# Optimization experiments

Measured on AMD Instinct MI355X. Metric: run time of the kernel, lower is better.

Reference implementation:

```python
import jax, jax.numpy as jnp
import numpy as np

B, L, D = 2, 4096, 128      # batch, seq_len, d_model
ED = 2 * D                  # d_inner (expand=2) = 256
N = 16                      # d_state
K = 4                       # d_conv
R = (D + 15) // 16          # dt_rank = 8
H = 2 * D                   # mlp hidden = 256


def setup_inputs() -> dict:
    key = jax.random.key(0)
    ks = jax.random.split(key, 20)
    s = 0.05
    inp = {
        "x": jax.random.normal(ks[0], (B, L, D), dtype=jnp.float32),
        # outer block LayerNorm (norm1)
        "norm1_g": jnp.ones((D,), jnp.float32),
        "norm1_b": jnp.zeros((D,), jnp.float32),
        # MambaLayer inner LayerNorm
        "inner_g": jnp.ones((D,), jnp.float32),
        "inner_b": jnp.zeros((D,), jnp.float32),
        # Mamba params
        "in_w": jax.random.normal(ks[1], (2 * ED, D), jnp.float32) * s,      # in_proj (no bias)
        "conv_w": jax.random.normal(ks[2], (ED, 1, K), jnp.float32) * s,     # depthwise conv
        "conv_b": jax.random.normal(ks[3], (ED,), jnp.float32) * s,
        "xproj_w": jax.random.normal(ks[4], (R + 2 * N, ED), jnp.float32) * s,  # x_proj (no bias)
        "dt_w": jax.random.normal(ks[5], (ED, R), jnp.float32) * s,
        "dt_b": jax.random.normal(ks[6], (ED,), jnp.float32) * s,
        "A_log": jnp.tile(jnp.log(jnp.arange(1, N + 1, dtype=jnp.float32)), (ED, 1)),  # [ED,N]
        "Dp": jnp.ones((ED,), jnp.float32),
        "out_w": jax.random.normal(ks[7], (D, ED), jnp.float32) * s,         # out_proj (no bias)
        # MLP
        "fc1_w": jax.random.normal(ks[8], (H, D), jnp.float32) * s,
        "fc1_b": jnp.zeros((H,), jnp.float32),
        "fc2_w": jax.random.normal(ks[9], (D, H), jnp.float32) * s,
        "fc2_b": jnp.zeros((D,), jnp.float32),
    }
    return inp


def _ln(x, g, b, eps=1e-5):
    m = jnp.mean(x, axis=-1, keepdims=True)
    v = jnp.mean((x - m) ** 2, axis=-1, keepdims=True)
    return (x - m) * jax.lax.rsqrt(v + eps) * g + b


def _mamba(x, in_w, conv_w, conv_b, xproj_w, dt_w, dt_b, A_log, Dp, out_w):
    # x: [B, L, D]
    xz = jnp.einsum('bld,ed->ble', x, in_w)          # [B,L,2*ED]
    u, z = jnp.split(xz, 2, axis=-1)                 # each [B,L,ED]
    # causal depthwise conv1d over L
    u_c = jnp.transpose(u, (0, 2, 1))                # [B,ED,L]
    u_c = jax.lax.conv_general_dilated(
        u_c, conv_w, window_strides=(1,), padding=[(K - 1, 0)],
        dimension_numbers=('NCH', 'OIH', 'NCH'), feature_group_count=ED)
    u = jax.nn.silu(jnp.transpose(u_c, (0, 2, 1)) + conv_b)   # [B,L,ED]
    # input-dependent dt, B, C
    dbc = jnp.einsum('ble,re->blr', u, xproj_w)      # [B,L,R+2N]
    dt, Bm, Cm = jnp.split(dbc, [R, R + N], axis=-1)
    delta = jax.nn.softplus(jnp.einsum('blr,er->ble', dt, dt_w) + dt_b)  # [B,L,ED]
    A = -jnp.exp(A_log)                              # [ED,N]
    deltaA = jnp.exp(jnp.einsum('ble,en->blen', delta, A))               # [B,L,ED,N]
    deltaBu = jnp.einsum('ble,bln,ble->blen', delta, Bm, u)              # [B,L,ED,N]
    # selective scan over L
    def step(h, inp):
        dA, dBu, Ct = inp                            # [B,ED,N],[B,ED,N],[B,N]
        h = dA * h + dBu
        y = jnp.einsum('ben,bn->be', h, Ct)
        return h, y
    h0 = jnp.zeros((B, ED, N), u.dtype)
    xs = (jnp.transpose(deltaA, (1, 0, 2, 3)),
          jnp.transpose(deltaBu, (1, 0, 2, 3)),
          jnp.transpose(Cm, (1, 0, 2)))
    _, ys = jax.lax.scan(step, h0, xs)               # [L,B,ED]
    y = jnp.transpose(ys, (1, 0, 2)) + u * Dp        # [B,L,ED]
    y = y * jax.nn.silu(z)
    return jnp.einsum('ble,de->bld', y, out_w)       # [B,L,D]


def reference(x, norm1_g, norm1_b, inner_g, inner_b, in_w, conv_w, conv_b,
              xproj_w, dt_w, dt_b, A_log, Dp, out_w, fc1_w, fc1_b, fc2_w, fc2_b):
    # attn branch: mamba(inner_LN(norm1(x)))
    a = _mamba(_ln(_ln(x, norm1_g, norm1_b), inner_g, inner_b),
               in_w, conv_w, conv_b, xproj_w, dt_w, dt_b, A_log, Dp, out_w)
    x = x + a
    # mlp branch (note: original applies norm1 again to updated x)
    h = _ln(x, norm1_g, norm1_b)
    h = jax.nn.gelu(jnp.einsum('bld,hd->blh', h, fc1_w) + fc1_b, approximate=False)
    h = jnp.einsum('blh,dh->bld', h, fc2_w) + fc2_b
    return x + h
```

## Files before the change

### kernel.cpp

```cpp
#include <hip/hip_runtime.h>
#include <hip/hip_bf16.h>
#include <math.h>

#define BB 2
#define LL 4096
#define DD 128
#define ED 256
#define NN 16
#define KK 4
#define RR 8
#define HH 256
#define NT (BB*LL)
#define NC 128
#define LC 32

typedef __attribute__((ext_vector_type(8))) short short8;
typedef __attribute__((ext_vector_type(8))) unsigned short ushort8v;
typedef __attribute__((ext_vector_type(4))) float floatx4;

__device__ __forceinline__ unsigned short f2bf(float f) {
  unsigned int b = __builtin_bit_cast(unsigned int, f);
  b += 0x7FFFu + ((b >> 16) & 1u);
  return (unsigned short)(b >> 16);
}

__global__ __launch_bounds__(256) void cvt5_k(const float* __restrict__ a,
    const float* __restrict__ b, const float* __restrict__ c,
    const float* __restrict__ d, const float* __restrict__ e5,
    unsigned short* __restrict__ oa, unsigned short* __restrict__ ob,
    unsigned short* __restrict__ oc, unsigned short* __restrict__ od,
    unsigned short* __restrict__ oe) {
  const int i = blockIdx.x*256 + threadIdx.x;
  const float* src; unsigned short* dst; int off;
  if (i < 16384)      { src = a;  dst = oa; off = i; }
  else if (i < 24576) { src = b;  dst = ob; off = i - 16384; }
  else if (i < 32768) { src = c;  dst = oc; off = i - 24576; }
  else if (i < 40960) { src = d;  dst = od; off = i - 32768; }
  else                { src = e5; dst = oe; off = i - 40960; }
  const float4 v = ((const float4*)src)[off];
  unsigned int lo = f2bf(v.x) | ((unsigned int)f2bf(v.y) << 16);
  unsigned int hi = f2bf(v.z) | ((unsigned int)f2bf(v.w) << 16);
  ((uint2*)dst)[off] = make_uint2(lo, hi);
}

__global__ __launch_bounds__(256) void gemm_inln_k(const float* __restrict__ x,
    const float* __restrict__ g1, const float* __restrict__ b1,
    const float* __restrict__ g2, const float* __restrict__ b2,
    const unsigned short* __restrict__ W, float* __restrict__ C) {
  __shared__ unsigned short As[64][136];
  __shared__ unsigned short Ws[64][136];
  const int row0 = blockIdx.y * 64;
  const int col0 = blockIdx.x * 64;
  const int tid  = threadIdx.x;
  const int wave = tid >> 6, lane = tid & 63;
  const int quad = lane >> 4, l16 = lane & 15;
  const int wm = (wave & 1) * 32, wn = (wave >> 1) * 32;
  const int lr = tid >> 2;
  const int lk = (tid & 3) * 32;

  {
    const float* Ap = x + (size_t)(row0 + lr)*DD + lk;
    float4 av[8];
    float s = 0.f, sq = 0.f;
    #pragma unroll
    for (int g = 0; g < 8; g++) {
      av[g] = *(const float4*)(Ap + g*4);
      s  += av[g].x + av[g].y + av[g].z + av[g].w;
      sq += av[g].x*av[g].x + av[g].y*av[g].y + av[g].z*av[g].z + av[g].w*av[g].w;
    }
    s += __shfl_xor(s, 1);  s += __shfl_xor(s, 2);
    sq += __shfl_xor(sq, 1); sq += __shfl_xor(sq, 2);
    const float m1 = s * (1.f/128.f);
    const float rs1 = rsqrtf(sq*(1.f/128.f) - m1*m1 + 1e-5f);
    float s2 = 0.f, sq2 = 0.f;
    #pragma unroll
    for (int g = 0; g < 8; g++) {
      const float4 gg = *(const float4*)(g1 + lk + g*4);
      const float4 bb = *(const float4*)(b1 + lk + g*4);
      av[g].x = (av[g].x - m1)*rs1*gg.x + bb.x;
      av[g].y = (av[g].y - m1)*rs1*gg.y + bb.y;
      av[g].z = (av[g].z - m1)*rs1*gg.z + bb.z;
      av[g].w = (av[g].w - m1)*rs1*gg.w + bb.w;
      s2  += av[g].x + av[g].y + av[g].z + av[g].w;
      sq2 += av[g].x*av[g].x + av[g].y*av[g].y + av[g].z*av[g].z + av[g].w*av[g].w;
    }
    s2 += __shfl_xor(s2, 1);  s2 += __shfl_xor(s2, 2);
    sq2 += __shfl_xor(sq2, 1); sq2 += __shfl_xor(sq2, 2);
    const float m2 = s2 * (1.f/128.f);
    const float rs2 = rsqrtf(sq2*(1.f/128.f) - m2*m2 + 1e-5f);
    #pragma unroll
    for (int g = 0; g < 4; g++) {
      const float4 ga = *(const float4*)(g2 + lk + g*8);
      const float4 gb = *(const float4*)(g2 + lk + g*8 + 4);
      const float4 ba = *(const float4*)(b2 + lk + g*8);
      const float4 bbv= *(const float4*)(b2 + lk + g*8 + 4);
      ushort8v pa;
      pa[0] = f2bf((av[2*g].x   - m2)*rs2*ga.x + ba.x);
      pa[1] = f2bf((av[2*g].y   - m2)*rs2*ga.y + ba.y);
      pa[2] = f2bf((av[2*g].z   - m2)*rs2*ga.z + ba.z);
      pa[3] = f2bf((av[2*g].w   - m2)*rs2*ga.w + ba.w);
      pa[4] = f2bf((av[2*g+1].x - m2)*rs2*gb.x + bbv.x);
      pa[5] = f2bf((av[2*g+1].y - m2)*rs2*gb.y + bbv.y);
      pa[6] = f2bf((av[2*g+1].z - m2)*rs2*gb.z + bbv.z);
      pa[7] = f2bf((av[2*g+1].w - m2)*rs2*gb.w + bbv.w);
      *(ushort8v*)&As[lr][lk + g*8] = pa;
    }
  }
  {
    const unsigned short* Wp = W + (size_t)(col0 + lr)*DD + lk;
    #pragma unroll
    for (int g = 0; g < 4; g++)
      *(ushort8v*)&Ws[lr][lk + g*8] = *(const ushort8v*)(Wp + g*8);
  }
  __syncthreads();

  floatx4 acc[2][2] = {};
  #pragma unroll
  for (int ks = 0; ks < 4; ks++) {
    const int ko = ks*32 + quad*8;
    short8 a0 = *(const short8*)&As[wm +      l16][ko];
    short8 a1 = *(const short8*)&As[wm + 16 + l16][ko];
    short8 b0 = *(const short8*)&Ws[wn +      l16][ko];
    short8 b1 = *(const short8*)&Ws[wn + 16 + l16][ko];
    acc[0][0] = __builtin_amdgcn_mfma_f32_16x16x32_bf16(a0, b0, acc[0][0], 0, 0, 0);
    acc[0][1] = __builtin_amdgcn_mfma_f32_16x16x32_bf16(a0, b1, acc[0][1], 0, 0, 0);
    acc[1][0] = __builtin_amdgcn_mfma_f32_16x16x32_bf16(a1, b0, acc[1][0], 0, 0, 0);
    acc[1][1] = __builtin_amdgcn_mfma_f32_16x16x32_bf16(a1, b1, acc[1][1], 0, 0, 0);
  }
  #pragma unroll
  for (int i = 0; i < 2; i++)
    #pragma unroll
    for (int j = 0; j < 2; j++) {
      const int n = col0 + wn + j*16 + l16;
      #pragma unroll
      for (int r = 0; r < 4; r++) {
        const int m = row0 + wm + i*16 + quad*4 + r;
        C[(size_t)m*(2*ED) + n] = acc[i][j][r];
      }
    }
}

template<int KD, int EPI, typename OT>
__global__ __launch_bounds__(256) void gemm_bf_k(
    const unsigned short* __restrict__ A, const unsigned short* __restrict__ W,
    const float* __restrict__ bias, const float* __restrict__ res,
    OT* __restrict__ C, int Nn) {
  static_assert(KD % 128 == 0, "KD multiple of 128");
  __shared__ unsigned short As[64][136];
  __shared__ unsigned short Ws[64][136];
  const int row0 = blockIdx.y * 64;
  const int col0 = blockIdx.x * 64;
  const int tid  = threadIdx.x;
  const int wave = tid >> 6, lane = tid & 63;
  const int quad = lane >> 4, l16 = lane & 15;
  const int wm = (wave & 1) * 32, wn = (wave >> 1) * 32;
  const int lr = tid >> 2, lc = (tid & 3) * 32;

  floatx4 acc[2][2] = {};
  for (int ks0 = 0; ks0 < KD; ks0 += 128) {
    const unsigned short* Ap = A + (size_t)(row0 + lr)*KD + ks0 + lc;
    const unsigned short* Wp = W + (size_t)(col0 + lr)*KD + ks0 + lc;
    ushort8v av[4], wv[4];
    #pragma unroll
    for (int g = 0; g < 4; g++) {
      av[g] = *(const ushort8v*)(Ap + g*8);
      wv[g] = *(const ushort8v*)(Wp + g*8);
    }
    __syncthreads();
    #pragma unroll
    for (int g = 0; g < 4; g++) {
      *(ushort8v*)&As[lr][lc + g*8] = av[g];
      *(ushort8v*)&Ws[lr][lc + g*8] = wv[g];
    }
    __syncthreads();
    #pragma unroll
    for (int ks = 0; ks < 4; ks++) {
      const int ko = ks*32 + quad*8;
      short8 a0 = *(const short8*)&As[wm +      l16][ko];
      short8 a1 = *(const short8*)&As[wm + 16 + l16][ko];
      short8 b0 = *(const short8*)&Ws[wn +      l16][ko];
      short8 b1 = *(const short8*)&Ws[wn + 16 + l16][ko];
      acc[0][0] = __builtin_amdgcn_mfma_f32_16x16x32_bf16(a0, b0, acc[0][0], 0, 0, 0);
      acc[0][1] = __builtin_amdgcn_mfma_f32_16x16x32_bf16(a0, b1, acc[0][1], 0, 0, 0);
      acc[1][0] = __builtin_amdgcn_mfma_f32_16x16x32_bf16(a1, b0, acc[1][0], 0, 0, 0);
      acc[1][1] = __builtin_amdgcn_mfma_f32_16x16x32_bf16(a1, b1, acc[1][1], 0, 0, 0);
    }
  }
  #pragma unroll
  for (int i = 0; i < 2; i++)
    #pragma unroll
    for (int j = 0; j < 2; j++) {
      const int n = col0 + wn + j*16 + l16;
      const float bn = bias[n];
      #pragma unroll
      for (int r = 0; r < 4; r++) {
        const int m = row0 + wm + i*16 + quad*4 + r;
        float v = acc[i][j][r] + bn;
        if constexpr (EPI == 2) v = 0.5f*v*(1.f + erff(v*0.70710678118f));
        const size_t o = (size_t)m*Nn + n;
        if constexpr (EPI == 3) v += res[o];
        if constexpr (sizeof(OT) == 2) C[o] = (OT)f2bf(v);
        else                           C[o] = v;
      }
    }
}

__global__ __launch_bounds__(256) void scan1f_k(
    const float* __restrict__ xz, const float* __restrict__ cw,
    const float* __restrict__ cb, const unsigned short* __restrict__ xpwb,
    const float* __restrict__ dtw, const float* __restrict__ dtb,
    const float* __restrict__ A_log, float* __restrict__ uc,
    float* __restrict__ dbc, float* __restrict__ delta,
    float* __restrict__ cA, float* __restrict__ cH) {
  __shared__ __align__(16) unsigned short Bs[64][264];
  __shared__ __align__(16) unsigned short As[32][264];
  __shared__ float su[32][128];
  __shared__ float sdbc[32][40];
  float (*sdel)[128] = reinterpret_cast<float(*)[128]>(&As[0][0]);

  const int eb = blockIdx.x, c = blockIdx.y, b = blockIdx.z;
  const int tid = threadIdx.x;
  const int t0 = b*LL + c*LC;

  #pragma unroll
  for (int p = 0; p < 8; p++) {
    const int idx = p*256 + tid;
    const int row = idx >> 5;
    const int col = (idx & 31) * 8;
    ushort8v v = {};
    if (row < 40) v = *(const ushort8v*)(xpwb + row*ED + col);
    *(ushort8v*)&Bs[row][col] = v;
  }

  {
    const int ch = tid;
    const float4 w = *(const float4*)(cw + ch*4);
    const float cbe = cb[ch];
    float h0 = 0.f, h1 = 0.f, h2 = 0.f;
    if (c != 0) {
      h0 = xz[(size_t)(t0-3)*(2*ED) + ch];
      h1 = xz[(size_t)(t0-2)*(2*ED) + ch];
      h2 = xz[(size_t)(t0-1)*(2*ED) + ch];
    }
    const bool own = (ch >> 7) == eb;
    #pragma unroll 8
    for (int i = 0; i < LC; i++) {
      const float cur = xz[(size_t)(t0+i)*(2*ED) + ch];
      const float a = cbe + h0*w.x + h1*w.y + h2*w.z + cur*w.w;
      const float s = a / (1.f + __expf(-a));
      As[i][ch] = f2bf(s);
      if (own) {
        su[i][ch & 127] = s;
        uc[(size_t)(t0+i)*ED + ch] = s;
      }
      h0 = h1; h1 = h2; h2 = cur;
    }
  }
  __syncthreads();

  const int wave = tid >> 6, lane = tid & 63;
  const int quad = lane >> 4, l16 = lane & 15;
  {
    const int mi = (wave & 1) * 16;
    const int j0 = (wave >> 1) * 2;
    floatx4 acc[2] = {};
    #pragma unroll
    for (int ks = 0; ks < 8; ks++) {
      const int ko = ks*32 + quad*8;
      short8 a  = *(const short8*)&As[mi + l16][ko];
      short8 b0 = *(const short8*)&Bs[j0*16 +      l16][ko];
      short8 b1 = *(const short8*)&Bs[j0*16 + 16 + l16][ko];
      acc[0] = __builtin_amdgcn_mfma_f32_16x16x32_bf16(a, b0, acc[0], 0, 0, 0);
      acc[1] = __builtin_amdgcn_mfma_f32_16x16x32_bf16(a, b1, acc[1], 0, 0, 0);
    }
    __syncthreads();
    #pragma unroll
    for (int f = 0; f < 2; f++) {
      const int n = (j0 + f)*16 + l16;
      #pragma unroll
      for (int r = 0; r < 4; r++) {
        const int m = mi + quad*4 + r;
        if (n < 40) {
          sdbc[m][n] = acc[f][r];
          if (eb == 0) dbc[(size_t)(t0 + m)*40 + n] = acc[f][r];
        }
      }
    }
  }
  __syncthreads();

  const int e_loc = tid >> 1;
  const int half  = tid & 1;
  const int e     = eb*128 + e_loc;
  {
    const float4 w0 = *(const float4*)(dtw + e*RR);
    const float4 w1 = *(const float4*)(dtw + e*RR + 4);
    const float db = dtb[e];
    #pragma unroll 4
    for (int i = 0; i < 16; i++) {
      const int t = half*16 + i;
      const float a = db
          + sdbc[t][0]*w0.x + sdbc[t][1]*w0.y + sdbc[t][2]*w0.z + sdbc[t][3]*w0.w
          + sdbc[t][4]*w1.x + sdbc[t][5]*w1.y + sdbc[t][6]*w1.z + sdbc[t][7]*w1.w;
      const float d = (a > 20.f) ? a : log1pf(__expf(a));
      sdel[t][e_loc] = d;
      delta[(size_t)(t0+t)*ED + e] = d;
    }
  }
  __syncthreads();

  const int n0 = half * 8;
  const float4 a0 = *(const float4*)(A_log + e*NN + n0);
  const float4 a1 = *(const float4*)(A_log + e*NN + n0 + 4);
  float Aen[8] = {-__expf(a0.x), -__expf(a0.y), -__expf(a0.z), -__expf(a0.w),
                  -__expf(a1.x), -__expf(a1.y), -__expf(a1.z), -__expf(a1.w)};
  float h[8] = {};
  float sumd = 0.f;
  for (int i = 0; i < LC; i++) {
    const float dv = sdel[i][e_loc];
    const float du = dv * su[i][e_loc];
    const float4 B0 = *(const float4*)&sdbc[i][RR + n0];
    const float4 B1 = *(const float4*)&sdbc[i][RR + n0 + 4];
    const float Bv[8] = {B0.x,B0.y,B0.z,B0.w,B1.x,B1.y,B1.z,B1.w};
    sumd += dv;
    #pragma unroll
    for (int j = 0; j < 8; j++)
      h[j] = __expf(dv * Aen[j])*h[j] + Bv[j]*du;
  }
  const size_t base = (((size_t)c*BB + b)*ED + e)*NN + n0;
  *(float4*)(cA + base)     = make_float4(__expf(sumd*Aen[0]), __expf(sumd*Aen[1]),
                                          __expf(sumd*Aen[2]), __expf(sumd*Aen[3]));
  *(float4*)(cA + base + 4) = make_float4(__expf(sumd*Aen[4]), __expf(sumd*Aen[5]),
                                          __expf(sumd*Aen[6]), __expf(sumd*Aen[7]));
  *(float4*)(cH + base)     = make_float4(h[0], h[1], h[2], h[3]);
  *(float4*)(cH + base + 4) = make_float4(h[4], h[5], h[6], h[7]);
}

__global__ __launch_bounds__(256) void scan2_k(float* __restrict__ cA,
    const float* __restrict__ cH) {
  const int gt = blockIdx.x*256 + threadIdx.x;
  const int b = gt >> 12;
  const size_t base = (size_t)b*ED*NN + (gt & 4095);
  float h = 0.f;
  for (int c = 0; c < NC; c++) {
    const size_t idx = (size_t)c*(BB*ED*NN) + base;
    const float a = cA[idx], hh = cH[idx];
    cA[idx] = h;
    h = a*h + hh;
  }
}

__global__ __launch_bounds__(256) void scan3_k(const float* __restrict__ delta,
    const float* __restrict__ uc, const float* __restrict__ dbc,
    const float* __restrict__ xz, const float* __restrict__ A_log,
    const float* __restrict__ Dpv, const float* __restrict__ cP,
    unsigned short* __restrict__ ybf) {
  const int c = blockIdx.y, b = blockIdx.z;
  const int e    = blockIdx.x*128 + (threadIdx.x >> 1);
  const int half = threadIdx.x & 1;
  const int n0   = half * 8;
  const float4 a0 = *(const float4*)(A_log + e*NN + n0);
  const float4 a1 = *(const float4*)(A_log + e*NN + n0 + 4);
  float Aen[8] = {-__expf(a0.x), -__expf(a0.y), -__expf(a0.z), -__expf(a0.w),
                  -__expf(a1.x), -__expf(a1.y), -__expf(a1.z), -__expf(a1.w)};
  const float Dpe = Dpv[e];
  const size_t base = (((size_t)c*BB + b)*ED + e)*NN + n0;
  const float4 h0 = *(const float4*)(cP + base);
  const float4 h1 = *(const float4*)(cP + base + 4);
  float h[8] = {h0.x,h0.y,h0.z,h0.w,h1.x,h1.y,h1.z,h1.w};
  const size_t tok0 = (size_t)b*LL + (size_t)c*LC;
  for (int i = 0; i < LC; i++) {
    const size_t t = tok0 + i;
    const float dv = delta[t*ED + e];
    const float uv = uc[t*ED + e];
    const float du = dv * uv;
    const float4 B0 = *(const float4*)(dbc + t*40 + RR + n0);
    const float4 B1 = *(const float4*)(dbc + t*40 + RR + n0 + 4);
    const float4 C0 = *(const float4*)(dbc + t*40 + RR + NN + n0);
    const float4 C1 = *(const float4*)(dbc + t*40 + RR + NN + n0 + 4);
    const float Bv[8] = {B0.x,B0.y,B0.z,B0.w,B1.x,B1.y,B1.z,B1.w};
    const float Cv[8] = {C0.x,C0.y,C0.z,C0.w,C1.x,C1.y,C1.z,C1.w};
    float part = 0.f;
    #pragma unroll
    for (int j = 0; j < 8; j++) {
      h[j] = __expf(dv * Aen[j])*h[j] + Bv[j]*du;
      part += h[j]*Cv[j];
    }
    part += __shfl_xor(part, 1);
    if (half == 0) {
      const float zv = xz[t*(2*ED) + ED + e];
      const float g = zv / (1.f + __expf(-zv));
      ybf[t*ED + e] = f2bf((part + uv*Dpe) * g);
    }
  }
}

__global__ __launch_bounds__(256) void gemm_outln_k(
    const unsigned short* __restrict__ A, const unsigned short* __restrict__ W,
    const float* __restrict__ xres, const float* __restrict__ g1,
    const float* __restrict__ b1, float* __restrict__ xnew,
    unsigned short* __restrict__ hlnbf) {
  __shared__ unsigned short As[32][136];
  __shared__ unsigned short Ws[128][136];
  __shared__ float xs[32][132];
  const int row0 = blockIdx.x * 32;
  const int tid  = threadIdx.x;
  const int wave = tid >> 6, lane = tid & 63;
  const int quad = lane >> 4, l16 = lane & 15;
  const int wm = (wave & 1) * 16;
  const int wn = (wave >> 1) * 64;

  floatx4 acc[4] = {};
  for (int ks0 = 0; ks0 < ED; ks0 += 128) {
    const int lr = tid >> 3, lk = (tid & 7) * 16;
    ushort8v a0 = *(const ushort8v*)(A + (size_t)(row0 + lr)*ED + ks0 + lk);
    ushort8v a1 = *(const ushort8v*)(A + (size_t)(row0 + lr)*ED + ks0 + lk + 8);
    const int wr = tid >> 1, wk = (tid & 1) * 64;
    ushort8v wv[8];
    #pragma unroll
    for (int g = 0; g < 8; g++)
      wv[g] = *(const ushort8v*)(W + (size_t)wr*ED + ks0 + wk + g*8);
    __syncthreads();
    *(ushort8v*)&As[lr][lk]     = a0;
    *(ushort8v*)&As[lr][lk + 8] = a1;
    #pragma unroll
    for (int g = 0; g < 8; g++) *(ushort8v*)&Ws[wr][wk + g*8] = wv[g];
    __syncthreads();
    #pragma unroll
    for (int ks = 0; ks < 4; ks++) {
      const int ko = ks*32 + quad*8;
      short8 a = *(const short8*)&As[wm + l16][ko];
      #pragma unroll
      for (int f = 0; f < 4; f++) {
        short8 b = *(const short8*)&Ws[wn + f*16 + l16][ko];
        acc[f] = __builtin_amdgcn_mfma_f32_16x16x32_bf16(a, b, acc[f], 0, 0, 0);
      }
    }
  }
  #pragma unroll
  for (int f = 0; f < 4; f++) {
    const int n = wn + f*16 + l16;
    #pragma unroll
    for (int r = 0; r < 4; r++) {
      const int m = wm + quad*4 + r;
      xs[m][n] = acc[f][r] + xres[(size_t)(row0 + m)*DD + n];
    }
  }
  __syncthreads();
  {
    const int lr = tid >> 3, le = (tid & 7) * 16;
    float vv[16];
    float s = 0.f, sq = 0.f;
    #pragma unroll
    for (int i = 0; i < 16; i++) {
      vv[i] = xs[lr][le + i];
      s += vv[i]; sq += vv[i]*vv[i];
    }
    s += __shfl_xor(s, 1);  s += __shfl_xor(s, 2);  s += __shfl_xor(s, 4);
    sq += __shfl_xor(sq, 1); sq += __shfl_xor(sq, 2); sq += __shfl_xor(sq, 4);
    const float mean = s * (1.f/128.f);
    const float rs = rsqrtf(sq*(1.f/128.f) - mean*mean + 1e-5f);
    const size_t ro = (size_t)(row0 + lr)*DD + le;
    #pragma unroll
    for (int g = 0; g < 4; g++)
      *(float4*)(xnew + ro + g*4) = make_float4(vv[4*g], vv[4*g+1], vv[4*g+2], vv[4*g+3]);
    #pragma unroll
    for (int g = 0; g < 2; g++) {
      ushort8v p;
      #pragma unroll
      for (int i = 0; i < 8; i++) {
        const int idx = g*8 + i;
        p[i] = f2bf((vv[idx] - mean)*rs*g1[le + idx] + b1[le + idx]);
      }
      *(ushort8v*)(hlnbf + ro + g*8) = p;
    }
  }
}

extern "C" void kernel_launch(void* const* d_in, const int* in_sizes, int n_in,
                              void* d_out, int out_size, void* d_ws, size_t ws_size,
                              hipStream_t stream) {
  const float* x      = (const float*)d_in[0];
  const float* n1g    = (const float*)d_in[1];
  const float* n1b    = (const float*)d_in[2];
  const float* ing    = (const float*)d_in[3];
  const float* inb    = (const float*)d_in[4];
  const float* in_w   = (const float*)d_in[5];
  const float* conv_w = (const float*)d_in[6];
  const float* conv_b = (const float*)d_in[7];
  const float* xproj_w= (const float*)d_in[8];
  const float* dt_w   = (const float*)d_in[9];
  const float* dt_b   = (const float*)d_in[10];
  const float* A_log  = (const float*)d_in[11];
  const float* Dpv    = (const float*)d_in[12];
  const float* out_w  = (const float*)d_in[13];
  const float* fc1_w  = (const float*)d_in[14];
  const float* fc1_b  = (const float*)d_in[15];
  const float* fc2_w  = (const float*)d_in[16];
  const float* fc2_b  = (const float*)d_in[17];
  float* out = (float*)d_out;

  float* ws    = (float*)d_ws;
  float* xz    = ws;
  float* uc    = xz    + (size_t)NT*2*ED;
  float* dbc   = uc    + (size_t)NT*ED;
  float* delta = dbc   + (size_t)NT*40;
  float* cAP   = delta + (size_t)NT*ED;
  float* cH    = cAP   + (size_t)NC*BB*ED*NN;
  float* xnew  = cH    + (size_t)NC*BB*ED*NN;
  unsigned short* ybf   = (unsigned short*)(xnew + (size_t)NT*DD);
  unsigned short* hlnbf = ybf   + (size_t)NT*ED;
  unsigned short* hmlbf = hlnbf + (size_t)NT*DD;
  unsigned short* wbin  = hmlbf + (size_t)NT*HH;
  unsigned short* wbout = wbin  + (size_t)2*ED*DD;
  unsigned short* wbf1  = wbout + (size_t)DD*ED;
  unsigned short* wbf2  = wbf1  + (size_t)HH*DD;
  unsigned short* wbxp  = wbf2  + (size_t)DD*HH;

  cvt5_k<<<170, 256, 0, stream>>>(in_w, out_w, fc1_w, fc2_w, xproj_w,
                                  wbin, wbout, wbf1, wbf2, wbxp);
  gemm_inln_k<<<dim3(512/64, NT/64), 256, 0, stream>>>(x, n1g, n1b, ing, inb, wbin, xz);
  scan1f_k<<<dim3(2, NC, BB), 256, 0, stream>>>(xz, conv_w, conv_b, wbxp, dt_w, dt_b,
                                                A_log, uc, dbc, delta, cAP, cH);
  scan2_k<<<(BB*ED*NN)/256, 256, 0, stream>>>(cAP, cH);
  scan3_k<<<dim3(2, NC, BB), 256, 0, stream>>>(delta, uc, dbc, xz, A_log, Dpv, cAP, ybf);
  gemm_outln_k<<<NT/32, 256, 0, stream>>>(ybf, wbout, x, n1g, n1b, xnew, hlnbf);
  gemm_bf_k<DD,2,unsigned short><<<dim3(HH/64, NT/64), 256, 0, stream>>>(hlnbf, wbf1, fc1_b, nullptr, hmlbf, HH);
  gemm_bf_k<HH,3,float><<<dim3(DD/64, NT/64), 256, 0, stream>>>(hmlbf, wbf2, fc2_b, xnew, out, DD);
}
```

Baseline: 198.3 us.

## Fuse scan output, out_proj, LayerNorm and MLP into one per-chunk tail kernel

Replaces scan3, the out_proj+LN GEMM and both MLP GEMMs with a single kernel per (chunk, batch). Each block holds its 32-token tile in shared memory across all stages and stages each weight matrix from fp32 to bf16 per block, so the ybf, xnew, hlnbf and hmlbf intermediates no longer go through global memory. The separate weight-conversion kernel is removed, and scan2 loads are batched 16 at a time. In exchange the tail grid has only 256 blocks at one block per CU with 256 threads each, each thread scans all 16 states serially, and every block re-converts the weights.

```diff
diff --git a/kernel.cpp b/kernel.cpp
--- a/kernel.cpp
+++ b/kernel.cpp
@@ -24,29 +24,17 @@
   return (unsigned short)(b >> 16);
 }
 
-__global__ __launch_bounds__(256) void cvt5_k(const float* __restrict__ a,
-    const float* __restrict__ b, const float* __restrict__ c,
-    const float* __restrict__ d, const float* __restrict__ e5,
-    unsigned short* __restrict__ oa, unsigned short* __restrict__ ob,
-    unsigned short* __restrict__ oc, unsigned short* __restrict__ od,
-    unsigned short* __restrict__ oe) {
-  const int i = blockIdx.x*256 + threadIdx.x;
-  const float* src; unsigned short* dst; int off;
-  if (i < 16384)      { src = a;  dst = oa; off = i; }
-  else if (i < 24576) { src = b;  dst = ob; off = i - 16384; }
-  else if (i < 32768) { src = c;  dst = oc; off = i - 24576; }
-  else if (i < 40960) { src = d;  dst = od; off = i - 32768; }
-  else                { src = e5; dst = oe; off = i - 40960; }
-  const float4 v = ((const float4*)src)[off];
-  unsigned int lo = f2bf(v.x) | ((unsigned int)f2bf(v.y) << 16);
-  unsigned int hi = f2bf(v.z) | ((unsigned int)f2bf(v.w) << 16);
-  ((uint2*)dst)[off] = make_uint2(lo, hi);
+__device__ __forceinline__ ushort8v pack8(const float4& v0, const float4& v1) {
+  ushort8v p;
+  p[0]=f2bf(v0.x); p[1]=f2bf(v0.y); p[2]=f2bf(v0.z); p[3]=f2bf(v0.w);
+  p[4]=f2bf(v1.x); p[5]=f2bf(v1.y); p[6]=f2bf(v1.z); p[7]=f2bf(v1.w);
+  return p;
 }
 
 __global__ __launch_bounds__(256) void gemm_inln_k(const float* __restrict__ x,
     const float* __restrict__ g1, const float* __restrict__ b1,
     const float* __restrict__ g2, const float* __restrict__ b2,
-    const unsigned short* __restrict__ W, float* __restrict__ C) {
+    const float* __restrict__ W, float* __restrict__ C) {
   __shared__ unsigned short As[64][136];
   __shared__ unsigned short Ws[64][136];
   const int row0 = blockIdx.y * 64;
@@ -107,10 +95,13 @@
     }
   }
   {
-    const unsigned short* Wp = W + (size_t)(col0 + lr)*DD + lk;
-    #pragma unroll
-    for (int g = 0; g < 4; g++)
-      *(ushort8v*)&Ws[lr][lk + g*8] = *(const ushort8v*)(Wp + g*8);
+    const float* Wp = W + (size_t)(col0 + lr)*DD + lk;
+    #pragma unroll
+    for (int g = 0; g < 4; g++) {
+      const float4 v0 = *(const float4*)(Wp + g*8);
+      const float4 v1 = *(const float4*)(Wp + g*8 + 4);
+      *(ushort8v*)&Ws[lr][lk + g*8] = pack8(v0, v1);
+    }
   }
   __syncthreads();
 
@@ -140,74 +131,9 @@
     }
 }
 
-template<int KD, int EPI, typename OT>
-__global__ __launch_bounds__(256) void gemm_bf_k(
-    const unsigned short* __restrict__ A, const unsigned short* __restrict__ W,
-    const float* __restrict__ bias, const float* __restrict__ res,
-    OT* __restrict__ C, int Nn) {
-  static_assert(KD % 128 == 0, "KD multiple of 128");
-  __shared__ unsigned short As[64][136];
-  __shared__ unsigned short Ws[64][136];
-  const int row0 = blockIdx.y * 64;
-  const int col0 = blockIdx.x * 64;
-  const int tid  = threadIdx.x;
-  const int wave = tid >> 6, lane = tid & 63;
-  const int quad = lane >> 4, l16 = lane & 15;
-  const int wm = (wave & 1) * 32, wn = (wave >> 1) * 32;
-  const int lr = tid >> 2, lc = (tid & 3) * 32;
-
-  floatx4 acc[2][2] = {};
-  for (int ks0 = 0; ks0 < KD; ks0 += 128) {
-    const unsigned short* Ap = A + (size_t)(row0 + lr)*KD + ks0 + lc;
-    const unsigned short* Wp = W + (size_t)(col0 + lr)*KD + ks0 + lc;
-    ushort8v av[4], wv[4];
-    #pragma unroll
-    for (int g = 0; g < 4; g++) {
-      av[g] = *(const ushort8v*)(Ap + g*8);
-      wv[g] = *(const ushort8v*)(Wp + g*8);
-    }
-    __syncthreads();
-    #pragma unroll
-    for (int g = 0; g < 4; g++) {
-      *(ushort8v*)&As[lr][lc + g*8] = av[g];
-      *(ushort8v*)&Ws[lr][lc + g*8] = wv[g];
-    }
-    __syncthreads();
-    #pragma unroll
-    for (int ks = 0; ks < 4; ks++) {
-      const int ko = ks*32 + quad*8;
-      short8 a0 = *(const short8*)&As[wm +      l16][ko];
-      short8 a1 = *(const short8*)&As[wm + 16 + l16][ko];
-      short8 b0 = *(const short8*)&Ws[wn +      l16][ko];
-      short8 b1 = *(const short8*)&Ws[wn + 16 + l16][ko];
-      acc[0][0] = __builtin_amdgcn_mfma_f32_16x16x32_bf16(a0, b0, acc[0][0], 0, 0, 0);
-      acc[0][1] = __builtin_amdgcn_mfma_f32_16x16x32_bf16(a0, b1, acc[0][1], 0, 0, 0);
-      acc[1][0] = __builtin_amdgcn_mfma_f32_16x16x32_bf16(a1, b0, acc[1][0], 0, 0, 0);
-      acc[1][1] = __builtin_amdgcn_mfma_f32_16x16x32_bf16(a1, b1, acc[1][1], 0, 0, 0);
-    }
-  }
-  #pragma unroll
-  for (int i = 0; i < 2; i++)
-    #pragma unroll
-    for (int j = 0; j < 2; j++) {
-      const int n = col0 + wn + j*16 + l16;
-      const float bn = bias[n];
-      #pragma unroll
-      for (int r = 0; r < 4; r++) {
-        const int m = row0 + wm + i*16 + quad*4 + r;
-        float v = acc[i][j][r] + bn;
-        if constexpr (EPI == 2) v = 0.5f*v*(1.f + erff(v*0.70710678118f));
-        const size_t o = (size_t)m*Nn + n;
-        if constexpr (EPI == 3) v += res[o];
-        if constexpr (sizeof(OT) == 2) C[o] = (OT)f2bf(v);
-        else                           C[o] = v;
-      }
-    }
-}
-
 __global__ __launch_bounds__(256) void scan1f_k(
     const float* __restrict__ xz, const float* __restrict__ cw,
-    const float* __restrict__ cb, const unsigned short* __restrict__ xpwb,
+    const float* __restrict__ cb, const float* __restrict__ xpw,
     const float* __restrict__ dtw, const float* __restrict__ dtb,
     const float* __restrict__ A_log, float* __restrict__ uc,
     float* __restrict__ dbc, float* __restrict__ delta,
@@ -228,7 +154,11 @@
     const int row = idx >> 5;
     const int col = (idx & 31) * 8;
     ushort8v v = {};
-    if (row < 40) v = *(const ushort8v*)(xpwb + row*ED + col);
+    if (row < 40) {
+      const float4 v0 = *(const float4*)(xpw + (size_t)row*ED + col);
+      const float4 v1 = *(const float4*)(xpw + (size_t)row*ED + col + 4);
+      v = pack8(v0, v1);
+    }
     *(ushort8v*)&Bs[row][col] = v;
   }
 
@@ -342,111 +272,119 @@
   const int b = gt >> 12;
   const size_t base = (size_t)b*ED*NN + (gt & 4095);
   float h = 0.f;
-  for (int c = 0; c < NC; c++) {
-    const size_t idx = (size_t)c*(BB*ED*NN) + base;
-    const float a = cA[idx], hh = cH[idx];
-    cA[idx] = h;
-    h = a*h + hh;
-  }
-}
-
-__global__ __launch_bounds__(256) void scan3_k(const float* __restrict__ delta,
+  for (int g = 0; g < NC/16; g++) {
+    float av[16], hv[16];
+    #pragma unroll
+    for (int i = 0; i < 16; i++) {
+      const size_t idx = (size_t)(g*16 + i)*(BB*ED*NN) + base;
+      av[i] = cA[idx]; hv[i] = cH[idx];
+    }
+    #pragma unroll
+    for (int i = 0; i < 16; i++) {
+      const size_t idx = (size_t)(g*16 + i)*(BB*ED*NN) + base;
+      cA[idx] = h;
+      h = av[i]*h + hv[i];
+    }
+  }
+}
+
+__global__ __launch_bounds__(256, 1) void tail_k(
+    const float* __restrict__ xz, const float* __restrict__ delta,
     const float* __restrict__ uc, const float* __restrict__ dbc,
-    const float* __restrict__ xz, const float* __restrict__ A_log,
-    const float* __restrict__ Dpv, const float* __restrict__ cP,
-    unsigned short* __restrict__ ybf) {
-  const int c = blockIdx.y, b = blockIdx.z;
-  const int e    = blockIdx.x*128 + (threadIdx.x >> 1);
-  const int half = threadIdx.x & 1;
-  const int n0   = half * 8;
-  const float4 a0 = *(const float4*)(A_log + e*NN + n0);
-  const float4 a1 = *(const float4*)(A_log + e*NN + n0 + 4);
-  float Aen[8] = {-__expf(a0.x), -__expf(a0.y), -__expf(a0.z), -__expf(a0.w),
-                  -__expf(a1.x), -__expf(a1.y), -__expf(a1.z), -__expf(a1.w)};
-  const float Dpe = Dpv[e];
-  const size_t base = (((size_t)c*BB + b)*ED + e)*NN + n0;
-  const float4 h0 = *(const float4*)(cP + base);
-  const float4 h1 = *(const float4*)(cP + base + 4);
-  float h[8] = {h0.x,h0.y,h0.z,h0.w,h1.x,h1.y,h1.z,h1.w};
-  const size_t tok0 = (size_t)b*LL + (size_t)c*LC;
-  for (int i = 0; i < LC; i++) {
-    const size_t t = tok0 + i;
-    const float dv = delta[t*ED + e];
-    const float uv = uc[t*ED + e];
-    const float du = dv * uv;
-    const float4 B0 = *(const float4*)(dbc + t*40 + RR + n0);
-    const float4 B1 = *(const float4*)(dbc + t*40 + RR + n0 + 4);
-    const float4 C0 = *(const float4*)(dbc + t*40 + RR + NN + n0);
-    const float4 C1 = *(const float4*)(dbc + t*40 + RR + NN + n0 + 4);
-    const float Bv[8] = {B0.x,B0.y,B0.z,B0.w,B1.x,B1.y,B1.z,B1.w};
-    const float Cv[8] = {C0.x,C0.y,C0.z,C0.w,C1.x,C1.y,C1.z,C1.w};
-    float part = 0.f;
-    #pragma unroll
-    for (int j = 0; j < 8; j++) {
-      h[j] = __expf(dv * Aen[j])*h[j] + Bv[j]*du;
-      part += h[j]*Cv[j];
-    }
-    part += __shfl_xor(part, 1);
-    if (half == 0) {
-      const float zv = xz[t*(2*ED) + ED + e];
-      const float g = zv / (1.f + __expf(-zv));
-      ybf[t*ED + e] = f2bf((part + uv*Dpe) * g);
-    }
-  }
-}
-
-__global__ __launch_bounds__(256) void gemm_outln_k(
-    const unsigned short* __restrict__ A, const unsigned short* __restrict__ W,
-    const float* __restrict__ xres, const float* __restrict__ g1,
-    const float* __restrict__ b1, float* __restrict__ xnew,
-    unsigned short* __restrict__ hlnbf) {
-  __shared__ unsigned short As[32][136];
-  __shared__ unsigned short Ws[128][136];
+    const float* __restrict__ cP, const float* __restrict__ A_log,
+    const float* __restrict__ Dpv, const float* __restrict__ x,
+    const float* __restrict__ g1, const float* __restrict__ b1,
+    const float* __restrict__ out_w, const float* __restrict__ fc1_w,
+    const float* __restrict__ fc1_b, const float* __restrict__ fc2_w,
+    const float* __restrict__ fc2_b, float* __restrict__ out) {
+  __shared__ __align__(16) unsigned short BigW[34816];
+  __shared__ __align__(16) unsigned short Au[32][264];
   __shared__ float xs[32][132];
-  const int row0 = blockIdx.x * 32;
-  const int tid  = threadIdx.x;
+  __shared__ float sbc[32][32];
+
+  const int c = blockIdx.x, b = blockIdx.y;
+  const int t0 = b*LL + c*LC;
+  const int tid = threadIdx.x;
   const int wave = tid >> 6, lane = tid & 63;
   const int quad = lane >> 4, l16 = lane & 15;
-  const int wm = (wave & 1) * 16;
-  const int wn = (wave >> 1) * 64;
-
-  floatx4 acc[4] = {};
-  for (int ks0 = 0; ks0 < ED; ks0 += 128) {
-    const int lr = tid >> 3, lk = (tid & 7) * 16;
-    ushort8v a0 = *(const ushort8v*)(A + (size_t)(row0 + lr)*ED + ks0 + lk);
-    ushort8v a1 = *(const ushort8v*)(A + (size_t)(row0 + lr)*ED + ks0 + lk + 8);
-    const int wr = tid >> 1, wk = (tid & 1) * 64;
-    ushort8v wv[8];
-    #pragma unroll
-    for (int g = 0; g < 8; g++)
-      wv[g] = *(const ushort8v*)(W + (size_t)wr*ED + ks0 + wk + g*8);
+
+  #pragma unroll
+  for (int p = 0; p < 4; p++) {
+    const int idx = p*256 + tid;
+    const int row = idx >> 5, col = idx & 31;
+    sbc[row][col] = dbc[(size_t)(t0 + row)*40 + RR + col];
+  }
+
+  {
+    const int e = tid;
+    float Aen[16], h[16];
+    #pragma unroll
+    for (int g = 0; g < 4; g++) {
+      const float4 a = *(const float4*)(A_log + e*NN + g*4);
+      Aen[4*g]=-__expf(a.x); Aen[4*g+1]=-__expf(a.y);
+      Aen[4*g+2]=-__expf(a.z); Aen[4*g+3]=-__expf(a.w);
+      const float4 hp = *(const float4*)(cP + (((size_t)c*BB + b)*ED + e)*NN + g*4);
+      h[4*g]=hp.x; h[4*g+1]=hp.y; h[4*g+2]=hp.z; h[4*g+3]=hp.w;
+    }
+    const float Dpe = Dpv[e];
     __syncthreads();
-    *(ushort8v*)&As[lr][lk]     = a0;
-    *(ushort8v*)&As[lr][lk + 8] = a1;
-    #pragma unroll
-    for (int g = 0; g < 8; g++) *(ushort8v*)&Ws[wr][wk + g*8] = wv[g];
-    __syncthreads();
-    #pragma unroll
-    for (int ks = 0; ks < 4; ks++) {
+    #pragma unroll 4
+    for (int i = 0; i < LC; i++) {
+      const float dv = delta[(size_t)(t0+i)*ED + e];
+      const float uv = uc[(size_t)(t0+i)*ED + e];
+      const float du = dv * uv;
+      float part = 0.f;
+      #pragma unroll
+      for (int j = 0; j < 16; j++) {
+        h[j] = __expf(dv * Aen[j])*h[j] + sbc[i][j]*du;
+        part += h[j]*sbc[i][16+j];
+      }
+      const float zv = xz[(size_t)(t0+i)*(2*ED) + ED + e];
+      const float g = zv / (1.f + __expf(-zv));
+      Au[i][e] = f2bf((part + uv*Dpe) * g);
+    }
+  }
+  {
+    const int r = tid >> 1, k0 = (tid & 1) * 128;
+    const float* wp = out_w + (size_t)r*ED + k0;
+    #pragma unroll
+    for (int g = 0; g < 16; g++) {
+      const float4 v0 = *(const float4*)(wp + g*8);
+      const float4 v1 = *(const float4*)(wp + g*8 + 4);
+      *(ushort8v*)&BigW[(size_t)r*264 + k0 + g*8] = pack8(v0, v1);
+    }
+  }
+  __syncthreads();
+
+  {
+    const int wn = wave * 32;
+    floatx4 acc[2][2] = {};
+    #pragma unroll
+    for (int ks = 0; ks < 8; ks++) {
       const int ko = ks*32 + quad*8;
-      short8 a = *(const short8*)&As[wm + l16][ko];
-      #pragma unroll
-      for (int f = 0; f < 4; f++) {
-        short8 b = *(const short8*)&Ws[wn + f*16 + l16][ko];
-        acc[f] = __builtin_amdgcn_mfma_f32_16x16x32_bf16(a, b, acc[f], 0, 0, 0);
-      }
-    }
-  }
-  #pragma unroll
-  for (int f = 0; f < 4; f++) {
-    const int n = wn + f*16 + l16;
-    #pragma unroll
-    for (int r = 0; r < 4; r++) {
-      const int m = wm + quad*4 + r;
-      xs[m][n] = acc[f][r] + xres[(size_t)(row0 + m)*DD + n];
-    }
-  }
-  __syncthreads();
+      short8 a0 = *(const short8*)&Au[l16][ko];
+      short8 a1 = *(const short8*)&Au[16 + l16][ko];
+      short8 b0 = *(const short8*)&BigW[(size_t)(wn +      l16)*264 + ko];
+      short8 b1 = *(const short8*)&BigW[(size_t)(wn + 16 + l16)*264 + ko];
+      acc[0][0] = __builtin_amdgcn_mfma_f32_16x16x32_bf16(a0, b0, acc[0][0], 0, 0, 0);
+      acc[0][1] = __builtin_amdgcn_mfma_f32_16x16x32_bf16(a0, b1, acc[0][1], 0, 0, 0);
+      acc[1][0] = __builtin_amdgcn_mfma_f32_16x16x32_bf16(a1, b0, acc[1][0], 0, 0, 0);
+      acc[1][1] = __builtin_amdgcn_mfma_f32_16x16x32_bf16(a1, b1, acc[1][1], 0, 0, 0);
+    }
+    #pragma unroll
+    for (int i = 0; i < 2; i++)
+      #pragma unroll
+      for (int j = 0; j < 2; j++) {
+        const int n = wn + j*16 + l16;
+        #pragma unroll
+        for (int r = 0; r < 4; r++) {
+          const int m = i*16 + quad*4 + r;
+          xs[m][n] = acc[i][j][r] + x[(size_t)(t0 + m)*DD + n];
+        }
+      }
+  }
+  __syncthreads();
+
   {
     const int lr = tid >> 3, le = (tid & 7) * 16;
     float vv[16];
@@ -460,10 +398,6 @@
     sq += __shfl_xor(sq, 1); sq += __shfl_xor(sq, 2); sq += __shfl_xor(sq, 4);
     const float mean = s * (1.f/128.f);
     const float rs = rsqrtf(sq*(1.f/128.f) - mean*mean + 1e-5f);
-    const size_t ro = (size_t)(row0 + lr)*DD + le;
-    #pragma unroll
-    for (int g = 0; g < 4; g++)
-      *(float4*)(xnew + ro + g*4) = make_float4(vv[4*g], vv[4*g+1], vv[4*g+2], vv[4*g+3]);
     #pragma unroll
     for (int g = 0; g < 2; g++) {
       ushort8v p;
@@ -472,8 +406,91 @@
         const int idx = g*8 + i;
         p[i] = f2bf((vv[idx] - mean)*rs*g1[le + idx] + b1[le + idx]);
       }
-      *(ushort8v*)(hlnbf + ro + g*8) = p;
-    }
+      *(ushort8v*)&Au[lr][le + g*8] = p;
+    }
+  }
+  {
+    const float* wp = fc1_w + (size_t)tid*DD;
+    #pragma unroll
+    for (int g = 0; g < 16; g++) {
+      const float4 v0 = *(const float4*)(wp + g*8);
+      const float4 v1 = *(const float4*)(wp + g*8 + 4);
+      *(ushort8v*)&BigW[(size_t)tid*136 + g*8] = pack8(v0, v1);
+    }
+  }
+  __syncthreads();
+
+  {
+    const int wn = wave * 64;
+    floatx4 acc[2][4] = {};
+    #pragma unroll
+    for (int ks = 0; ks < 4; ks++) {
+      const int ko = ks*32 + quad*8;
+      short8 a0 = *(const short8*)&Au[l16][ko];
+      short8 a1 = *(const short8*)&Au[16 + l16][ko];
+      #pragma unroll
+      for (int f = 0; f < 4; f++) {
+        short8 bv = *(const short8*)&BigW[(size_t)(wn + f*16 + l16)*136 + ko];
+        acc[0][f] = __builtin_amdgcn_mfma_f32_16x16x32_bf16(a0, bv, acc[0][f], 0, 0, 0);
+        acc[1][f] = __builtin_amdgcn_mfma_f32_16x16x32_bf16(a1, bv, acc[1][f], 0, 0, 0);
+      }
+    }
+    __syncthreads();
+    #pragma unroll
+    for (int i = 0; i < 2; i++)
+      #pragma unroll
+      for (int f = 0; f < 4; f++) {
+        const int n = wn + f*16 + l16;
+        const float bn = fc1_b[n];
+        #pragma unroll
+        for (int r = 0; r < 4; r++) {
+          const int m = i*16 + quad*4 + r;
+          float v = acc[i][f][r] + bn;
+          v = 0.5f*v*(1.f + erff(v*0.70710678118f));
+          Au[m][n] = f2bf(v);
+        }
+      }
+  }
+  {
+    const int r = tid >> 1, k0 = (tid & 1) * 128;
+    const float* wp = fc2_w + (size_t)r*HH + k0;
+    __syncthreads();
+    #pragma unroll
+    for (int g = 0; g < 16; g++) {
+      const float4 v0 = *(const float4*)(wp + g*8);
+      const float4 v1 = *(const float4*)(wp + g*8 + 4);
+      *(ushort8v*)&BigW[(size_t)r*264 + k0 + g*8] = pack8(v0, v1);
+    }
+  }
+  __syncthreads();
+
+  {
+    const int wn = wave * 32;
+    floatx4 acc[2][2] = {};
+    #pragma unroll
+    for (int ks = 0; ks < 8; ks++) {
+      const int ko = ks*32 + quad*8;
+      short8 a0 = *(const short8*)&Au[l16][ko];
+      short8 a1 = *(const short8*)&Au[16 + l16][ko];
+      short8 b0 = *(const short8*)&BigW[(size_t)(wn +      l16)*264 + ko];
+      short8 b1 = *(const short8*)&BigW[(size_t)(wn + 16 + l16)*264 + ko];
+      acc[0][0] = __builtin_amdgcn_mfma_f32_16x16x32_bf16(a0, b0, acc[0][0], 0, 0, 0);
+      acc[0][1] = __builtin_amdgcn_mfma_f32_16x16x32_bf16(a0, b1, acc[0][1], 0, 0, 0);
+      acc[1][0] = __builtin_amdgcn_mfma_f32_16x16x32_bf16(a1, b0, acc[1][0], 0, 0, 0);
+      acc[1][1] = __builtin_amdgcn_mfma_f32_16x16x32_bf16(a1, b1, acc[1][1], 0, 0, 0);
+    }
+    #pragma unroll
+    for (int i = 0; i < 2; i++)
+      #pragma unroll
+      for (int j = 0; j < 2; j++) {
+        const int n = wn + j*16 + l16;
+        const float bn = fc2_b[n];
+        #pragma unroll
+        for (int r = 0; r < 4; r++) {
+          const int m = i*16 + quad*4 + r;
+          out[(size_t)(t0 + m)*DD + n] = acc[i][j][r] + bn + xs[m][n];
+        }
+      }
   }
 }
 
@@ -507,24 +524,12 @@
   float* delta = dbc   + (size_t)NT*40;
   float* cAP   = delta + (size_t)NT*ED;
   float* cH    = cAP   + (size_t)NC*BB*ED*NN;
-  float* xnew  = cH    + (size_t)NC*BB*ED*NN;
-  unsigned short* ybf   = (unsigned short*)(xnew + (size_t)NT*DD);
-  unsigned short* hlnbf = ybf   + (size_t)NT*ED;
-  unsigned short* hmlbf = hlnbf + (size_t)NT*DD;
-  unsigned short* wbin  = hmlbf + (size_t)NT*HH;
-  unsigned short* wbout = wbin  + (size_t)2*ED*DD;
-  unsigned short* wbf1  = wbout + (size_t)DD*ED;
-  unsigned short* wbf2  = wbf1  + (size_t)HH*DD;
-  unsigned short* wbxp  = wbf2  + (size_t)DD*HH;
-
-  cvt5_k<<<170, 256, 0, stream>>>(in_w, out_w, fc1_w, fc2_w, xproj_w,
-                                  wbin, wbout, wbf1, wbf2, wbxp);
-  gemm_inln_k<<<dim3(512/64, NT/64), 256, 0, stream>>>(x, n1g, n1b, ing, inb, wbin, xz);
-  scan1f_k<<<dim3(2, NC, BB), 256, 0, stream>>>(xz, conv_w, conv_b, wbxp, dt_w, dt_b,
+
+  gemm_inln_k<<<dim3(512/64, NT/64), 256, 0, stream>>>(x, n1g, n1b, ing, inb, in_w, xz);
+  scan1f_k<<<dim3(2, NC, BB), 256, 0, stream>>>(xz, conv_w, conv_b, xproj_w, dt_w, dt_b,
                                                 A_log, uc, dbc, delta, cAP, cH);
   scan2_k<<<(BB*ED*NN)/256, 256, 0, stream>>>(cAP, cH);
-  scan3_k<<<dim3(2, NC, BB), 256, 0, stream>>>(delta, uc, dbc, xz, A_log, Dpv, cAP, ybf);
-  gemm_outln_k<<<NT/32, 256, 0, stream>>>(ybf, wbout, x, n1g, n1b, xnew, hlnbf);
-  gemm_bf_k<DD,2,unsigned short><<<dim3(HH/64, NT/64), 256, 0, stream>>>(hlnbf, wbf1, fc1_b, nullptr, hmlbf, HH);
-  gemm_bf_k<HH,3,float><<<dim3(DD/64, NT/64), 256, 0, stream>>>(hmlbf, wbf2, fc2_b, xnew, out, DD);
-}
+  tail_k<<<dim3(NC, BB), 256, 0, stream>>>(xz, delta, uc, dbc, cAP, A_log, Dpv,
+                                           x, n1g, n1b, out_w, fc1_w, fc1_b,
+                                           fc2_w, fc2_b, out);
+}
```

Measured after the change: 188.7 us. -4.8%, faster.
